# Optimization experiments

Hardware: AMD Instinct MI355X
Metric: run time of the kernel (lower is better)

## Reference

```python
import jax, jax.numpy as jnp
import numpy as np
from jax import lax

RADIUS = 2
DILATION = 2
KS = 2 * RADIUS + 1  # 5
PERM = np.array([6, 8, 1, 11, 2, 10, 0, 7, 9, 4, 5, 3])


def _shift_kernels():
    # Reproduce the torch index construction in numpy (all constants).
    six = np.array([[0, 1, 1], [1, 1, 0], [1, 0, 1], [1, 1, 2], [2, 1, 1], [1, 2, 1]])
    # pairwise squared distances between the 6 neighbourhood offsets
    d = ((six[:, None, :] - six[None, :, :]) ** 2).sum(-1)
    x, y = np.meshgrid(np.arange(6), np.arange(6), indexing='ij')
    mask = (x > y).reshape(-1) & (d == 2).reshape(-1)
    idx1 = np.repeat(six[:, None, :], 6, axis=1).reshape(-1, 3)[mask]
    idx2 = np.repeat(six[None, :, :], 6, axis=0).reshape(-1, 3)[mask]
    k1 = np.zeros((12, 1, 3, 3, 3), np.float32)
    k2 = np.zeros((12, 1, 3, 3, 3), np.float32)
    r = np.arange(12)
    k1[r, 0, idx1[:, 0], idx1[:, 1], idx1[:, 2]] = 1.0
    k2[r, 0, idx2[:, 0], idx2[:, 1], idx2[:, 2]] = 1.0
    return jnp.asarray(k1), jnp.asarray(k2)

_K1, _K2 = _shift_kernels()
DN = ('NCDHW', 'OIDHW', 'NCDHW')


def _rep_pad(x, p):
    return jnp.pad(x, ((0, 0), (0, 0), (p, p), (p, p), (p, p)), mode='edge')


def mindssc(img):
    # img: [N,1,D,H,W]
    p1 = _rep_pad(img, DILATION)
    c1 = lax.conv_general_dilated(p1, _K1, (1, 1, 1), 'VALID',
                                  rhs_dilation=(DILATION,) * 3, dimension_numbers=DN)
    c2 = lax.conv_general_dilated(p1, _K2, (1, 1, 1), 'VALID',
                                  rhs_dilation=(DILATION,) * 3, dimension_numbers=DN)
    diff2 = (c1 - c2) ** 2  # [N,12,D,H,W]
    p2 = _rep_pad(diff2, RADIUS)
    ssd = lax.reduce_window(p2, 0.0, lax.add, (1, 1, KS, KS, KS),
                            (1, 1, 1, 1, 1), 'VALID') / float(KS ** 3)
    mind = ssd - jnp.min(ssd, axis=1, keepdims=True)
    mind_var = jnp.mean(mind, axis=1, keepdims=True)
    m = jnp.mean(mind_var)
    mind_var = jnp.clip(mind_var, m * 0.001, m * 1000.0)
    mind = jnp.exp(-mind / mind_var)
    return mind[:, PERM]


def setup_inputs() -> dict:
    key = jax.random.key(0)
    k1, k2 = jax.random.split(key)
    shape = (1, 1, 128, 128, 128)
    return {
        'y_true': jax.random.normal(k1, shape, dtype=jnp.float32),
        'y_pred': jax.random.normal(k2, shape, dtype=jnp.float32),
    }


def reference(y_true, y_pred):
    return jnp.mean((mindssc(y_pred) - mindssc(y_true)) ** 2)
```

## Files before the change

kernel.cpp:

```cpp
#include <hip/hip_runtime.h>

#define DIM   128
#define DMASK 127
#define PLANE (DIM * DIM)
#define VOX   (1 << 21)
#define NCH   12

typedef __attribute__((ext_vector_type(2))) _Float16 half2v;

__constant__ int c_sd1[12] = { 0, 0, 0, 0, 0, 2, 2, 2, 0, 0, 0, 0};
__constant__ int c_sh1[12] = { 0,-2,-2, 0, 0, 0, 0, 0, 2, 2, 2, 2};
__constant__ int c_sw1[12] = {-2, 0, 0, 2, 2, 0, 0, 0, 0, 0, 0, 0};
__constant__ int c_sd2[12] = {-2,-2, 0,-2, 0, 0, 0, 0,-2, 0, 0, 2};
__constant__ int c_sh2[12] = { 0, 0, 0, 0,-2, 0,-2, 0, 0, 0, 0, 0};
__constant__ int c_sw2[12] = { 0, 0,-2, 0, 0,-2, 0, 2, 0,-2, 2, 0};

__device__ __forceinline__ int clamp7(int v) { return min(max(v, 0), DMASK); }


#define STREAM_PIPE(IMC, WIN, HIST, IMGI, S5C)                               \
    {                                                                        \
        float tX[8], tY[8];                                                  \
        _Pragma("unroll")                                                    \
        for (int r = 0; r < 8; ++r) {                                        \
            float2 a = *(const float2*)(IMC + (pOffA + rowOffA[r] + colA));  \
            float2 b = *(const float2*)(IMC + (pOffB + rowOffB[r] + colB));  \
            a.y = fixAlo ? a.x : a.y;  a.x = fixAhi ? a.y : a.x;             \
            b.y = fixBlo ? b.x : b.y;  b.x = fixBhi ? b.y : b.x;             \
            float dx = a.x - b.x; dx *= dx;                    \
            float dy = a.y - b.y; dy *= dy;                    \
            float lx = __shfl_up(dx, 1, 64);                   \
            float ly = __shfl_up(dy, 1, 64);                   \
            float rx = __shfl_down(dx, 1, 64);                 \
            float ry = __shfl_down(dy, 1, 64);                 \
            ly = (l == 0)  ? dx : ly;                    \
            rx = (l == 63) ? dy : rx;                    \
            float m = ly + dx + dy + rx;                                     \
            tX[r] = lx + m;                                 \
            tY[r] = m + ry;                                 \
        }                                                                    \
        float sx = tX[0] + tX[1] + tX[2] + tX[3] + tX[4];                    \
        float sy = tY[0] + tY[1] + tY[2] + tY[3] + tY[4];                    \
        _Pragma("unroll")                                                    \
        for (int k = 0; k < 4; ++k) {                                        \
            half2v hv = { (_Float16)sx, (_Float16)sy };     \
            half2v old = HIST[S5C][k];                                       \
            WIN[k].x += (float)hv[0] - (float)old[0];                        \
            WIN[k].y += (float)hv[1] - (float)old[1];                        \
            HIST[S5C][k] = hv;                                               \
            if (dowrite) {                                                   \
                half2v ov = { (_Float16)WIN[k].x, (_Float16)WIN[k].y };      \
                sb[bb][ch][IMGI][k][l] = ov;                                 \
            }                                                                \
            if (k < 3) {                                                     \
                sx += tX[k + 5] - tX[k];                                     \
                sy += tY[k + 5] - tY[k];                                     \
            }                                                                \
        }                                                                    \
    }

__global__ __launch_bounds__(768) void ffuse(const float* __restrict__ img0,
                                             const float* __restrict__ img1,
                                             float* __restrict__ partial) {
    __shared__ half2v sb[2][NCH][2][4][64];
    __shared__ float sred[4];

    int tid = threadIdx.x;
    int wv  = tid >> 6;
    int l   = tid & 63;

    int bx = blockIdx.x;
    int h0 = (bx & 31) << 2;
    int d0 = (bx >> 5) << 4;

    int ch = wv;
    int sd1 = c_sd1[ch], sh1 = c_sh1[ch], sw1 = c_sw1[ch];
    int sd2 = c_sd2[ch], sh2 = c_sh2[ch], sw2 = c_sw2[ch];

    int rowOffA[8], rowOffB[8];
#pragma unroll
    for (int r = 0; r < 8; ++r) {
        int hq = clamp7(h0 - 2 + r);
        rowOffA[r] = clamp7(hq + sh1) * (DIM * 4);
        rowOffB[r] = clamp7(hq + sh2) * (DIM * 4);
    }

    int c2 = l << 1;
    int colA = min(max(c2 + sw1, 0), 126) * 4;
    int colB = min(max(c2 + sw2, 0), 126) * 4;
    bool fixAlo = (sw1 < 0) && (l == 0);
    bool fixAhi = (sw1 > 0) && (l == 63);
    bool fixBlo = (sw2 < 0) && (l == 0);
    bool fixBhi = (sw2 > 0) && (l == 63);

    float2 win0[4], win1[4];
    half2v hist0[5][4], hist1[5][4];
#pragma unroll
    for (int k = 0; k < 4; ++k) {
        win0[k].x = 0.0f; win0[k].y = 0.0f;
        win1[k].x = 0.0f; win1[k].y = 0.0f;
#pragma unroll
        for (int s = 0; s < 5; ++s) {
            hist0[s][k] = half2v{(_Float16)0.0f, (_Float16)0.0f};
            hist1[s][k] = half2v{(_Float16)0.0f, (_Float16)0.0f};
        }
    }

    const char* im0 = (const char*)img0;
    const char* im1 = (const char*)img1;

    float acc = 0.0f;

    for (int oo = 0; oo < 4; ++oo) {
#pragma unroll
        for (int s5 = 0; s5 < 5; ++s5) {
            int it = oo * 5 + s5;
            int dp = clamp7(d0 - 2 + it);
            int pOffA = clamp7(dp + sd1) * (PLANE * 4);
            int pOffB = clamp7(dp + sd2) * (PLANE * 4);
            bool dowrite = (it >= 4);
            int bb = it & 1;

            STREAM_PIPE(im0, win0, hist0, 0, s5)
            STREAM_PIPE(im1, win1, hist1, 1, s5)

            if (dowrite) {
                __syncthreads();
                if (tid < 256) {
                    int rrow = wv;
                    float mn0x = 3.4e38f, mn0y = 3.4e38f, sm0x = 0.f, sm0y = 0.f;
                    float mn1x = 3.4e38f, mn1y = 3.4e38f, sm1x = 0.f, sm1y = 0.f;
#pragma unroll
                    for (int c = 0; c < 12; ++c) {
                        half2v h0 = sb[bb][c][0][rrow][l];
                        half2v h1 = sb[bb][c][1][rrow][l];
                        float v0x = (float)h0[0], v0y = (float)h0[1];
                        float v1x = (float)h1[0], v1y = (float)h1[1];
                        mn0x = fminf(mn0x, v0x); sm0x += v0x;
                        mn0y = fminf(mn0y, v0y); sm0y += v0y;
                        mn1x = fminf(mn1x, v1x); sm1x += v1x;
                        mn1y = fminf(mn1y, v1y); sm1y += v1y;
                    }
                    float i0x = __fdividef(1.0f, sm0x * (1.0f / 12.0f) - mn0x);
                    float i0y = __fdividef(1.0f, sm0y * (1.0f / 12.0f) - mn0y);
                    float i1x = __fdividef(1.0f, sm1x * (1.0f / 12.0f) - mn1x);
                    float i1y = __fdividef(1.0f, sm1y * (1.0f / 12.0f) - mn1y);
#pragma unroll
                    for (int c = 0; c < 12; ++c) {
                        half2v h0 = sb[bb][c][0][rrow][l];
                        half2v h1 = sb[bb][c][1][rrow][l];
                        float e0x = __expf(-((float)h0[0] - mn0x) * i0x);
                        float e1x = __expf(-((float)h1[0] - mn1x) * i1x);
                        float e0y = __expf(-((float)h0[1] - mn0y) * i0y);
                        float e1y = __expf(-((float)h1[1] - mn1y) * i1y);
                        float dfx = e0x - e1x, dfy = e0y - e1y;
                        acc += dfx * dfx + dfy * dfy;
                    }
                }
            }
        }
    }

    if (tid < 256) {
#pragma unroll
        for (int off = 32; off > 0; off >>= 1)
            acc += __shfl_down(acc, off, 64);
        if ((tid & 63) == 0) sred[tid >> 6] = acc;
    }
    __syncthreads();
    if (tid == 0)
        partial[blockIdx.x] = sred[0] + sred[1] + sred[2] + sred[3];
}

__global__ __launch_bounds__(256) void kred(const float* __restrict__ partial,
                                            float* __restrict__ out) {
    int tid = threadIdx.x;
    float acc = partial[tid];
#pragma unroll
    for (int off = 32; off > 0; off >>= 1)
        acc += __shfl_down(acc, off, 64);
    __shared__ float smem[4];
    int lane = tid & 63, wv = tid >> 6;
    if (lane == 0) smem[wv] = acc;
    __syncthreads();
    if (tid == 0)
        out[0] = (smem[0] + smem[1] + smem[2] + smem[3])
               * (1.0f / (12.0f * (float)VOX));
}

__global__ void kdiag(float* out, float ws_mb) { out[0] = ws_mb; }

extern "C" void kernel_launch(void* const* d_in, const int* in_sizes, int n_in,
                              void* d_out, int out_size, void* d_ws, size_t ws_size,
                              hipStream_t stream) {
    const float* y_true = (const float*)d_in[0];
    const float* y_pred = (const float*)d_in[1];
    float* out = (float*)d_out;

    const size_t NEED = 4096;
    if (ws_size < NEED) {
        kdiag<<<1, 1, 0, stream>>>(out, (float)(ws_size >> 20));
        return;
    }

    float* partial = (float*)d_ws;

    ffuse<<<dim3(256), 768, 0, stream>>>(y_true, y_pred, partial);
    kred<<<1, 256, 0, stream>>>(partial, out);
}
```

Before: 138.1 us.

## Halve depth per block, rotate epilogue across wave groups, use DPP lane shifts

```diff
diff --git a/kernel.cpp b/kernel.cpp
--- a/kernel.cpp
+++ b/kernel.cpp
@@ -16,6 +16,15 @@
 __constant__ int c_sw2[12] = { 0, 0,-2, 0, 0,-2, 0, 2, 0,-2, 2, 0};
 
 __device__ __forceinline__ int clamp7(int v) { return min(max(v, 0), DMASK); }
+
+__device__ __forceinline__ float dpp_shr1(float old_, float src) {
+    return __int_as_float(__builtin_amdgcn_update_dpp(
+        __float_as_int(old_), __float_as_int(src), 0x138, 0xF, 0xF, false));
+}
+__device__ __forceinline__ float dpp_shl1(float old_, float src) {
+    return __int_as_float(__builtin_amdgcn_update_dpp(
+        __float_as_int(old_), __float_as_int(src), 0x130, 0xF, 0xF, false));
+}
 
 
 #define STREAM_PIPE(IMC, WIN, HIST, IMGI, S5C)                               \
@@ -29,12 +38,10 @@
             b.y = fixBlo ? b.x : b.y;  b.x = fixBhi ? b.y : b.x;             \
             float dx = a.x - b.x; dx *= dx;                    \
             float dy = a.y - b.y; dy *= dy;                    \
-            float lx = __shfl_up(dx, 1, 64);                   \
-            float ly = __shfl_up(dy, 1, 64);                   \
-            float rx = __shfl_down(dx, 1, 64);                 \
-            float ry = __shfl_down(dy, 1, 64);                 \
-            ly = (l == 0)  ? dx : ly;                    \
-            rx = (l == 63) ? dy : rx;                    \
+            float lx = dpp_shr1(dx, dx);               \
+            float ly = dpp_shr1(dx, dy);               \
+            float rx = dpp_shl1(dy, dx);              \
+            float ry = dpp_shl1(dy, dy);              \
             float m = ly + dx + dy + rx;                                     \
             tX[r] = lx + m;                                 \
             tY[r] = m + ry;                                 \
@@ -59,11 +66,57 @@
         }                                                                    \
     }
 
-__global__ __launch_bounds__(768) void ffuse(const float* __restrict__ img0,
-                                             const float* __restrict__ img1,
-                                             float* __restrict__ partial) {
+#define PLANE_ITER(IT_EXPR, S5C)                                             \
+    {                                                                        \
+        int it = (IT_EXPR);                                                  \
+        int dp = clamp7(d0 - 2 + it);                                        \
+        int pOffA = clamp7(dp + sd1) * (PLANE * 4);                          \
+        int pOffB = clamp7(dp + sd2) * (PLANE * 4);                          \
+        bool dowrite = (it >= 4);                                            \
+        int bb = it & 1;                                                     \
+        STREAM_PIPE(im0, win0, hist0, 0, S5C)                                \
+        STREAM_PIPE(im1, win1, hist1, 1, S5C)                                \
+        if (dowrite) {                                                       \
+            __syncthreads();                                                 \
+            if ((wv >> 2) == ((it - 4) % 3)) {                               \
+                int rrow = wv & 3;                                           \
+                float mn0x = 3.4e38f, mn0y = 3.4e38f, sm0x = 0.f, sm0y = 0.f;\
+                float mn1x = 3.4e38f, mn1y = 3.4e38f, sm1x = 0.f, sm1y = 0.f;\
+                _Pragma("unroll")                                            \
+                for (int c = 0; c < 12; ++c) {                               \
+                    half2v g0 = sb[bb][c][0][rrow][l];                       \
+                    half2v g1 = sb[bb][c][1][rrow][l];                       \
+                    float v0x = (float)g0[0], v0y = (float)g0[1];            \
+                    float v1x = (float)g1[0], v1y = (float)g1[1];            \
+                    mn0x = fminf(mn0x, v0x); sm0x += v0x;                    \
+                    mn0y = fminf(mn0y, v0y); sm0y += v0y;                    \
+                    mn1x = fminf(mn1x, v1x); sm1x += v1x;                    \
+                    mn1y = fminf(mn1y, v1y); sm1y += v1y;                    \
+                }                                                            \
+                float i0x = __fdividef(1.0f, sm0x * (1.0f/12.0f) - mn0x);    \
+                float i0y = __fdividef(1.0f, sm0y * (1.0f/12.0f) - mn0y);    \
+                float i1x = __fdividef(1.0f, sm1x * (1.0f/12.0f) - mn1x);    \
+                float i1y = __fdividef(1.0f, sm1y * (1.0f/12.0f) - mn1y);    \
+                _Pragma("unroll")                                            \
+                for (int c = 0; c < 12; ++c) {                               \
+                    half2v g0 = sb[bb][c][0][rrow][l];                       \
+                    half2v g1 = sb[bb][c][1][rrow][l];                       \
+                    float e0x = __expf(-((float)g0[0] - mn0x) * i0x);        \
+                    float e1x = __expf(-((float)g1[0] - mn1x) * i1x);        \
+                    float e0y = __expf(-((float)g0[1] - mn0y) * i0y);        \
+                    float e1y = __expf(-((float)g1[1] - mn1y) * i1y);        \
+                    float dfx = e0x - e1x, dfy = e0y - e1y;                  \
+                    acc += dfx * dfx + dfy * dfy;                            \
+                }                                                            \
+            }                                                                \
+        }                                                                    \
+    }
+
+__global__ __launch_bounds__(768, 6) void ffuse(const float* __restrict__ img0,
+                                                const float* __restrict__ img1,
+                                                float* __restrict__ partial) {
     __shared__ half2v sb[2][NCH][2][4][64];
-    __shared__ float sred[4];
+    __shared__ float sred[12];
 
     int tid = threadIdx.x;
     int wv  = tid >> 6;
@@ -71,7 +124,7 @@
 
     int bx = blockIdx.x;
     int h0 = (bx & 31) << 2;
-    int d0 = (bx >> 5) << 4;
+    int d0 = (bx >> 5) << 3;
 
     int ch = wv;
     int sd1 = c_sd1[ch], sh1 = c_sh1[ch], sw1 = c_sw1[ch];
@@ -111,71 +164,33 @@
 
     float acc = 0.0f;
 
-    for (int oo = 0; oo < 4; ++oo) {
-#pragma unroll
-        for (int s5 = 0; s5 < 5; ++s5) {
-            int it = oo * 5 + s5;
-            int dp = clamp7(d0 - 2 + it);
-            int pOffA = clamp7(dp + sd1) * (PLANE * 4);
-            int pOffB = clamp7(dp + sd2) * (PLANE * 4);
-            bool dowrite = (it >= 4);
-            int bb = it & 1;
-
-            STREAM_PIPE(im0, win0, hist0, 0, s5)
-            STREAM_PIPE(im1, win1, hist1, 1, s5)
-
-            if (dowrite) {
-                __syncthreads();
-                if (tid < 256) {
-                    int rrow = wv;
-                    float mn0x = 3.4e38f, mn0y = 3.4e38f, sm0x = 0.f, sm0y = 0.f;
-                    float mn1x = 3.4e38f, mn1y = 3.4e38f, sm1x = 0.f, sm1y = 0.f;
-#pragma unroll
-                    for (int c = 0; c < 12; ++c) {
-                        half2v h0 = sb[bb][c][0][rrow][l];
-                        half2v h1 = sb[bb][c][1][rrow][l];
-                        float v0x = (float)h0[0], v0y = (float)h0[1];
-                        float v1x = (float)h1[0], v1y = (float)h1[1];
-                        mn0x = fminf(mn0x, v0x); sm0x += v0x;
-                        mn0y = fminf(mn0y, v0y); sm0y += v0y;
-                        mn1x = fminf(mn1x, v1x); sm1x += v1x;
-                        mn1y = fminf(mn1y, v1y); sm1y += v1y;
-                    }
-                    float i0x = __fdividef(1.0f, sm0x * (1.0f / 12.0f) - mn0x);
-                    float i0y = __fdividef(1.0f, sm0y * (1.0f / 12.0f) - mn0y);
-                    float i1x = __fdividef(1.0f, sm1x * (1.0f / 12.0f) - mn1x);
-                    float i1y = __fdividef(1.0f, sm1y * (1.0f / 12.0f) - mn1y);
-#pragma unroll
-                    for (int c = 0; c < 12; ++c) {
-                        half2v h0 = sb[bb][c][0][rrow][l];
-                        half2v h1 = sb[bb][c][1][rrow][l];
-                        float e0x = __expf(-((float)h0[0] - mn0x) * i0x);
-                        float e1x = __expf(-((float)h1[0] - mn1x) * i1x);
-                        float e0y = __expf(-((float)h0[1] - mn0y) * i0y);
-                        float e1y = __expf(-((float)h1[1] - mn1y) * i1y);
-                        float dfx = e0x - e1x, dfy = e0y - e1y;
-                        acc += dfx * dfx + dfy * dfy;
-                    }
-                }
-            }
-        }
-    }
-
-    if (tid < 256) {
-#pragma unroll
-        for (int off = 32; off > 0; off >>= 1)
-            acc += __shfl_down(acc, off, 64);
-        if ((tid & 63) == 0) sred[tid >> 6] = acc;
-    }
+#pragma unroll
+    for (int j = 0; j < 2; ++j)
+        PLANE_ITER(j, j)
+
+    for (int oo = 0; oo < 2; ++oo) {
+#pragma unroll
+        for (int j = 0; j < 5; ++j)
+            PLANE_ITER(2 + oo * 5 + j, ((2 + j) % 5))
+    }
+
+#pragma unroll
+    for (int off = 32; off > 0; off >>= 1)
+        acc += __shfl_down(acc, off, 64);
+    if (l == 0) sred[wv] = acc;
     __syncthreads();
-    if (tid == 0)
-        partial[blockIdx.x] = sred[0] + sred[1] + sred[2] + sred[3];
+    if (tid == 0) {
+        float s = 0.0f;
+#pragma unroll
+        for (int w = 0; w < 12; ++w) s += sred[w];
+        partial[blockIdx.x] = s;
+    }
 }
 
 __global__ __launch_bounds__(256) void kred(const float* __restrict__ partial,
                                             float* __restrict__ out) {
     int tid = threadIdx.x;
-    float acc = partial[tid];
+    float acc = partial[tid] + partial[tid + 256];
 #pragma unroll
     for (int off = 32; off > 0; off >>= 1)
         acc += __shfl_down(acc, off, 64);
@@ -205,6 +220,6 @@
 
     float* partial = (float*)d_ws;
 
-    ffuse<<<dim3(256), 768, 0, stream>>>(y_true, y_pred, partial);
+    ffuse<<<dim3(512), 768, 0, stream>>>(y_true, y_pred, partial);
     kred<<<1, 256, 0, stream>>>(partial, out);
 }
```

Result: slower. 234.1 us (+69.5%).

## Use DPP lane shifts for neighbor sums and rotate epilogue across wave groups

Applied to the files above, without the earlier changes.

```diff
diff --git a/kernel.cpp b/kernel.cpp
--- a/kernel.cpp
+++ b/kernel.cpp
@@ -16,6 +16,15 @@
 __constant__ int c_sw2[12] = { 0, 0,-2, 0, 0,-2, 0, 2, 0,-2, 2, 0};
 
 __device__ __forceinline__ int clamp7(int v) { return min(max(v, 0), DMASK); }
+
+__device__ __forceinline__ float dpp_shr1(float old_, float src) {
+    return __int_as_float(__builtin_amdgcn_update_dpp(
+        __float_as_int(old_), __float_as_int(src), 0x138, 0xF, 0xF, false));
+}
+__device__ __forceinline__ float dpp_shl1(float old_, float src) {
+    return __int_as_float(__builtin_amdgcn_update_dpp(
+        __float_as_int(old_), __float_as_int(src), 0x130, 0xF, 0xF, false));
+}
 
 
 #define STREAM_PIPE(IMC, WIN, HIST, IMGI, S5C)                               \
@@ -29,12 +38,10 @@
             b.y = fixBlo ? b.x : b.y;  b.x = fixBhi ? b.y : b.x;             \
             float dx = a.x - b.x; dx *= dx;                    \
             float dy = a.y - b.y; dy *= dy;                    \
-            float lx = __shfl_up(dx, 1, 64);                   \
-            float ly = __shfl_up(dy, 1, 64);                   \
-            float rx = __shfl_down(dx, 1, 64);                 \
-            float ry = __shfl_down(dy, 1, 64);                 \
-            ly = (l == 0)  ? dx : ly;                    \
-            rx = (l == 63) ? dy : rx;                    \
+            float lx = dpp_shr1(dx, dx);               \
+            float ly = dpp_shr1(dx, dy);               \
+            float rx = dpp_shl1(dy, dx);              \
+            float ry = dpp_shl1(dy, dy);              \
             float m = ly + dx + dy + rx;                                     \
             tX[r] = lx + m;                                 \
             tY[r] = m + ry;                                 \
@@ -63,7 +70,7 @@
                                              const float* __restrict__ img1,
                                              float* __restrict__ partial) {
     __shared__ half2v sb[2][NCH][2][4][64];
-    __shared__ float sred[4];
+    __shared__ float sred[12];
 
     int tid = threadIdx.x;
     int wv  = tid >> 6;
@@ -126,16 +133,16 @@
 
             if (dowrite) {
                 __syncthreads();
-                if (tid < 256) {
-                    int rrow = wv;
+                if ((wv >> 2) == ((it - 4) % 3)) {
+                    int rrow = wv & 3;
                     float mn0x = 3.4e38f, mn0y = 3.4e38f, sm0x = 0.f, sm0y = 0.f;
                     float mn1x = 3.4e38f, mn1y = 3.4e38f, sm1x = 0.f, sm1y = 0.f;
 #pragma unroll
                     for (int c = 0; c < 12; ++c) {
-                        half2v h0 = sb[bb][c][0][rrow][l];
-                        half2v h1 = sb[bb][c][1][rrow][l];
-                        float v0x = (float)h0[0], v0y = (float)h0[1];
-                        float v1x = (float)h1[0], v1y = (float)h1[1];
+                        half2v g0 = sb[bb][c][0][rrow][l];
+                        half2v g1 = sb[bb][c][1][rrow][l];
+                        float v0x = (float)g0[0], v0y = (float)g0[1];
+                        float v1x = (float)g1[0], v1y = (float)g1[1];
                         mn0x = fminf(mn0x, v0x); sm0x += v0x;
                         mn0y = fminf(mn0y, v0y); sm0y += v0y;
                         mn1x = fminf(mn1x, v1x); sm1x += v1x;
@@ -147,12 +154,12 @@
                     float i1y = __fdividef(1.0f, sm1y * (1.0f / 12.0f) - mn1y);
 #pragma unroll
                     for (int c = 0; c < 12; ++c) {
-                        half2v h0 = sb[bb][c][0][rrow][l];
-                        half2v h1 = sb[bb][c][1][rrow][l];
-                        float e0x = __expf(-((float)h0[0] - mn0x) * i0x);
-                        float e1x = __expf(-((float)h1[0] - mn1x) * i1x);
-                        float e0y = __expf(-((float)h0[1] - mn0y) * i0y);
-                        float e1y = __expf(-((float)h1[1] - mn1y) * i1y);
+                        half2v g0 = sb[bb][c][0][rrow][l];
+                        half2v g1 = sb[bb][c][1][rrow][l];
+                        float e0x = __expf(-((float)g0[0] - mn0x) * i0x);
+                        float e1x = __expf(-((float)g1[0] - mn1x) * i1x);
+                        float e0y = __expf(-((float)g0[1] - mn0y) * i0y);
+                        float e1y = __expf(-((float)g1[1] - mn1y) * i1y);
                         float dfx = e0x - e1x, dfy = e0y - e1y;
                         acc += dfx * dfx + dfy * dfy;
                     }
@@ -161,15 +168,17 @@
         }
     }
 
-    if (tid < 256) {
-#pragma unroll
-        for (int off = 32; off > 0; off >>= 1)
-            acc += __shfl_down(acc, off, 64);
-        if ((tid & 63) == 0) sred[tid >> 6] = acc;
-    }
+#pragma unroll
+    for (int off = 32; off > 0; off >>= 1)
+        acc += __shfl_down(acc, off, 64);
+    if (l == 0) sred[wv] = acc;
     __syncthreads();
-    if (tid == 0)
-        partial[blockIdx.x] = sred[0] + sred[1] + sred[2] + sred[3];
+    if (tid == 0) {
+        float s = 0.0f;
+#pragma unroll
+        for (int w = 0; w < 12; ++w) s += sred[w];
+        partial[blockIdx.x] = s;
+    }
 }
 
 __global__ __launch_bounds__(256) void kred(const float* __restrict__ partial,
```

Result: faster. 134.5 us (-2.6%).
